# Kernel optimization log

Measured on AMD Instinct MI355X. Metric: run time of the kernel, lower is better.

The kernel has to match this reference:

```python
import jax, jax.numpy as jnp
import numpy as np

N_NODES = 100000
NEG_SLOPE = 0.2  # PyG GATConv default


def gat_conv(x, src, dst, W, a_src, a_dst, n_nodes):
    """One PyG-style GATConv (with self-loops already appended to src/dst).
    x: [N, Fin], W: [Fin, H*C], a_src/a_dst: [H, C]. Returns [N, H, C]."""
    H, C = a_src.shape
    h = (x @ W).reshape(-1, H, C)                      # [N, H, C]
    s_src = jnp.einsum('nhc,hc->nh', h, a_src)         # [N, H]
    s_dst = jnp.einsum('nhc,hc->nh', h, a_dst)         # [N, H]
    e = jax.nn.leaky_relu(s_src[src] + s_dst[dst], NEG_SLOPE)  # [E, H]
    # segment softmax over incoming edges of each destination node
    e_max = jax.ops.segment_max(e, dst, num_segments=n_nodes)  # [N, H]
    e_exp = jnp.exp(e - e_max[dst])
    denom = jax.ops.segment_sum(e_exp, dst, num_segments=n_nodes)
    alpha = e_exp / (denom[dst] + 1e-16)               # [E, H]
    msg = h[src] * alpha[:, :, None]                   # [E, H, C]
    return jax.ops.segment_sum(msg, dst, num_segments=n_nodes)  # [N, H, C]


def setup_inputs() -> dict:
    key = jax.random.key(0)
    ks = jax.random.split(key, 10)
    in_dim, hidden, heads, out_dim = 128, 32, 4, 32
    N, E = N_NODES, 1600000
    x = jax.random.normal(ks[0], (N, in_dim), dtype=jnp.float32)
    edge_index = jax.random.randint(ks[1], (2, E), 0, N, dtype=jnp.int64)
    s = 0.1
    return {
        'x': x,
        'edge_index': edge_index,
        'W1': s * jax.random.normal(ks[2], (in_dim, heads * hidden), dtype=jnp.float32),
        'a_src1': s * jax.random.normal(ks[3], (heads, hidden), dtype=jnp.float32),
        'a_dst1': s * jax.random.normal(ks[4], (heads, hidden), dtype=jnp.float32),
        'b1': jnp.zeros((heads * hidden,), dtype=jnp.float32),
        'W2': s * jax.random.normal(ks[5], (heads * hidden, out_dim), dtype=jnp.float32),
        'a_src2': s * jax.random.normal(ks[6], (1, out_dim), dtype=jnp.float32),
        'a_dst2': s * jax.random.normal(ks[7], (1, out_dim), dtype=jnp.float32),
        'b2': jnp.zeros((out_dim,), dtype=jnp.float32),
    }


def reference(x, edge_index, W1, a_src1, a_dst1, b1, W2, a_src2, a_dst2, b2):
    N = x.shape[0]
    loops = jnp.arange(N, dtype=edge_index.dtype)
    src = jnp.concatenate([edge_index[0], loops])  # PyG adds self-loops
    dst = jnp.concatenate([edge_index[1], loops])
    h1 = gat_conv(x, src, dst, W1, a_src1, a_dst1, N)      # [N, H, C]
    h1 = jax.nn.elu(h1.reshape(N, -1) + b1)                # concat heads + bias, elu
    h2 = gat_conv(h1, src, dst, W2, a_src2, a_dst2, N)     # [N, 1, out]
    return h2.mean(axis=1) + b2                            # concat=False -> mean over heads
```

## Files before the change

kernel.cpp:

```cpp
#include <hip/hip_runtime.h>
#include <hip/hip_bf16.h>

#define NEG 0.2f
#define BK_SHIFT 9
#define BK_CAP 9216

typedef short short8 __attribute__((ext_vector_type(8)));
typedef float f32x4 __attribute__((ext_vector_type(4)));

__device__ __forceinline__ float lrelu(float x){ return x > 0.f ? x : NEG * x; }
__device__ __forceinline__ float elu_f(float x){ return x > 0.f ? x : expm1f(x); }
__device__ __forceinline__ unsigned short f2bf(float f){
  unsigned int u = __float_as_uint(f);
  unsigned int r = u + 0x7fffu + ((u >> 16) & 1u);
  return (unsigned short)(r >> 16);
}
__device__ __forceinline__ float bf2f(unsigned short u){
  return __uint_as_float(((unsigned int)u) << 16);
}

__global__ __launch_bounds__(256) void k_binA(
    const int* __restrict__ src, const int* __restrict__ dst, int E,
    int* __restrict__ gcursor, int2* __restrict__ ebuf){
  __shared__ int hist[256];
  __shared__ int base[256];
  int t = threadIdx.x;
  hist[t] = 0;
  __syncthreads();
  int e0 = blockIdx.x * 4096;
  for (int j = 0; j < 16; j++){
    int e = e0 + j * 256 + t;
    if (e < E) atomicAdd(&hist[dst[e] >> BK_SHIFT], 1);
  }
  __syncthreads();
  int cnt = hist[t];
  if (cnt > 0) base[t] = atomicAdd(&gcursor[t], cnt);
  hist[t] = 0;
  __syncthreads();
  for (int j = 0; j < 16; j++){
    int e = e0 + j * 256 + t;
    if (e < E){
      int d = dst[e]; int b = d >> BK_SHIFT;
      int loc = atomicAdd(&hist[b], 1);
      ebuf[(size_t)b * BK_CAP + base[b] + loc] = make_int2(src[e], d);
    }
  }
}

__global__ __launch_bounds__(256) void k_degB(
    const int2* __restrict__ ebuf, const int* __restrict__ gcount,
    int* __restrict__ deg, int N){
  __shared__ int ld[512];
  int b = blockIdx.x, t = threadIdx.x;
  ld[t] = 0; ld[t + 256] = 0;
  __syncthreads();
  int cnt = gcount[b];
  int nbase = b << BK_SHIFT;
  const int2* eb = ebuf + (size_t)b * BK_CAP;
  for (int i = t; i < cnt; i += 256)
    atomicAdd(&ld[eb[i].y - nbase], 1);
  __syncthreads();
  int n0 = nbase + t;
  if (n0 < N) deg[n0] = ld[t];
  int n1 = nbase + 256 + t;
  if (n1 < N) deg[n1] = ld[t + 256];
}

__global__ void k_scan1(const int* __restrict__ deg, int* row_ptr, int* partials, int N){
  __shared__ int sd[256];
  int t = threadIdx.x;
  int base = blockIdx.x * 1024 + t * 4;
  int v[4]; int s = 0;
  #pragma unroll
  for (int j = 0; j < 4; j++){ int i = base + j; v[j] = (i < N) ? (deg[i] + 1) : 0; s += v[j]; }
  sd[t] = s; __syncthreads();
  for (int off = 1; off < 256; off <<= 1){
    int x = (t >= off) ? sd[t - off] : 0;
    __syncthreads(); sd[t] += x; __syncthreads();
  }
  int pre = (t > 0) ? sd[t - 1] : 0;
  #pragma unroll
  for (int j = 0; j < 4; j++){ int i = base + j; if (i < N) row_ptr[i] = pre; pre += v[j]; }
  if (t == 255) partials[blockIdx.x] = sd[255];
}

__global__ void k_scan2(int* partials, int NB){
  __shared__ int sd[128];
  int t = threadIdx.x;
  int v = (t < NB) ? partials[t] : 0;
  sd[t] = v; __syncthreads();
  for (int off = 1; off < 128; off <<= 1){
    int x = (t >= off) ? sd[t - off] : 0;
    __syncthreads(); sd[t] += x; __syncthreads();
  }
  if (t < NB) partials[t] = sd[t] - v;
}

__global__ void k_scan3(int* row_ptr, const int* __restrict__ partials, int N, int total){
  int i = blockIdx.x * blockDim.x + threadIdx.x;
  if (i < N){ int r = row_ptr[i] + partials[i >> 10]; row_ptr[i] = r; }
  if (i == 0) row_ptr[N] = total;
}

__global__ __launch_bounds__(256) void k_csrB(
    const int2* __restrict__ ebuf, const int* __restrict__ gcount,
    const int* __restrict__ rowp, int* __restrict__ csr, int N){
  __shared__ int cur[512];
  int b = blockIdx.x, t = threadIdx.x;
  int nbase = b << BK_SHIFT;
  int n0 = nbase + t;
  int n1 = nbase + 256 + t;
  cur[t]       = (n0 < N) ? rowp[n0] : 0;
  cur[t + 256] = (n1 < N) ? rowp[n1] : 0;
  __syncthreads();
  int cnt = gcount[b];
  const int2* eb = ebuf + (size_t)b * BK_CAP;
  for (int i = t; i < cnt; i += 256){
    int2 e = eb[i];
    int pos = atomicAdd(&cur[e.y - nbase], 1);
    csr[pos] = e.x;
  }
  __syncthreads();
  if (n0 < N) csr[cur[t]] = n0;
  if (n1 < N) csr[cur[t + 256]] = n1;
}

__global__ __launch_bounds__(256, 3) void k_gemm1(
    const float* __restrict__ x, const float* __restrict__ W,
    unsigned short* __restrict__ h_bf, int N){
  __shared__ unsigned short Wt[128 * 136];
  __shared__ unsigned short Xb[64 * 136];
  int t = threadIdx.x;
  int rb = blockIdx.x * 64;

  {
    int n = t & 127, kh = (t >> 7) << 6;
    #pragma unroll
    for (int j = 0; j < 16; j++){
      int k0 = kh + j * 4;
      float w0 = W[(size_t)(k0 + 0) * 128 + n];
      float w1 = W[(size_t)(k0 + 1) * 128 + n];
      float w2 = W[(size_t)(k0 + 2) * 128 + n];
      float w3 = W[(size_t)(k0 + 3) * 128 + n];
      uint2 pk;
      pk.x = ((unsigned)f2bf(w1) << 16) | f2bf(w0);
      pk.y = ((unsigned)f2bf(w3) << 16) | f2bf(w2);
      *(uint2*)&Wt[n * 136 + k0] = pk;
    }
  }
  #pragma unroll
  for (int j = 0; j < 8; j++){
    int fi = j * 256 + t;
    int row = fi >> 5, k4 = (fi & 31) * 4;
    int gr = rb + row;
    float4 v = make_float4(0.f, 0.f, 0.f, 0.f);
    if (gr < N) v = *(const float4*)&x[(size_t)gr * 128 + k4];
    uint2 pk;
    pk.x = ((unsigned)f2bf(v.y) << 16) | f2bf(v.x);
    pk.y = ((unsigned)f2bf(v.w) << 16) | f2bf(v.z);
    *(uint2*)&Xb[row * 136 + k4] = pk;
  }
  __syncthreads();

  int w = t >> 6, l = t & 63;
  int m = l & 15, quad = l >> 4;
  f32x4 acc[8];
  #pragma unroll
  for (int ct = 0; ct < 8; ct++) acc[ct] = (f32x4){0.f, 0.f, 0.f, 0.f};

  #pragma unroll
  for (int kc = 0; kc < 4; kc++){
    short8 a = *(const short8*)&Xb[(w * 16 + m) * 136 + kc * 32 + quad * 8];
    #pragma unroll
    for (int ct = 0; ct < 8; ct++){
      short8 b = *(const short8*)&Wt[(ct * 16 + m) * 136 + kc * 32 + quad * 8];
      acc[ct] = __builtin_amdgcn_mfma_f32_16x16x32_bf16(a, b, acc[ct], 0, 0, 0);
    }
  }

  #pragma unroll
  for (int reg = 0; reg < 4; reg++){
    int gr = rb + w * 16 + quad * 4 + reg;
    if (gr < N){
      #pragma unroll
      for (int ct = 0; ct < 8; ct++)
        h_bf[(size_t)gr * 128 + ct * 16 + m] = f2bf(acc[ct][reg]);
    }
  }
}

__global__ __launch_bounds__(256) void k_score1(
    const unsigned int* __restrict__ hb, const float* __restrict__ a_src,
    const float* __restrict__ a_dst, float* __restrict__ ss, float* __restrict__ sd, int N){
  int n = blockIdx.x * 4 + (threadIdx.x >> 6);
  if (n >= N) return;
  int l = threadIdx.x & 63;
  unsigned int u = hb[(size_t)n * 64 + l];
  float vx = bf2f((unsigned short)(u & 0xffff));
  float vy = bf2f((unsigned short)(u >> 16));
  float ps = vx * a_src[2 * l] + vy * a_src[2 * l + 1];
  float pd = vx * a_dst[2 * l] + vy * a_dst[2 * l + 1];
  ps += __shfl_xor(ps, 1, 16); ps += __shfl_xor(ps, 2, 16);
  ps += __shfl_xor(ps, 4, 16); ps += __shfl_xor(ps, 8, 16);
  pd += __shfl_xor(pd, 1, 16); pd += __shfl_xor(pd, 2, 16);
  pd += __shfl_xor(pd, 4, 16); pd += __shfl_xor(pd, 8, 16);
  if ((l & 15) == 0){
    int hd = l >> 4;
    ss[(size_t)n * 4 + hd] = ps;
    sd[(size_t)n * 4 + hd] = pd;
  }
}

__global__ __launch_bounds__(256) void k_agg1(
    const int* __restrict__ row_ptr, const int* __restrict__ csr_src,
    const float* __restrict__ ss, const float* __restrict__ sdst,
    const __hip_bfloat162* __restrict__ hb2,
    unsigned int* __restrict__ out1_bf, int N){
  int n = blockIdx.x * 4 + (threadIdx.x >> 6);
  if (n >= N) return;
  int l = threadIdx.x & 63;
  int hd = l >> 4;
  int j4 = l & 3;
  int hh = (l >> 2) & 3;
  float swv = sdst[(size_t)n * 4 + hh];
  float sdv = sdst[(size_t)n * 4 + hd];
  int beg = row_ptr[n], end = row_ptr[n + 1];
  float ax = 0.f, ay = 0.f, sw = 0.f;
  int e = beg;
  for (; e + 4 <= end; e += 4){
    int sj = csr_src[e + j4];
    float wv = __expf(lrelu(ss[(size_t)sj * 4 + hh] + swv));
    int s0 = __shfl(sj, 0, 4), s1 = __shfl(sj, 1, 4);
    int s2 = __shfl(sj, 2, 4), s3 = __shfl(sj, 3, 4);
    float w0 = __shfl(wv, hd * 4 + 0, 16), w1 = __shfl(wv, hd * 4 + 1, 16);
    float w2 = __shfl(wv, hd * 4 + 2, 16), w3 = __shfl(wv, hd * 4 + 3, 16);
    float2 v0 = __bfloat1622float2(hb2[(size_t)s0 * 64 + l]);
    float2 v1 = __bfloat1622float2(hb2[(size_t)s1 * 64 + l]);
    float2 v2 = __bfloat1622float2(hb2[(size_t)s2 * 64 + l]);
    float2 v3 = __bfloat1622float2(hb2[(size_t)s3 * 64 + l]);
    ax += w0*v0.x + w1*v1.x + w2*v2.x + w3*v3.x;
    ay += w0*v0.y + w1*v1.y + w2*v2.y + w3*v3.y;
    sw += w0 + w1 + w2 + w3;
  }
  for (; e < end; e++){
    int s = csr_src[e];
    float w = __expf(lrelu(ss[(size_t)s * 4 + hd] + sdv));
    float2 v = __bfloat1622float2(hb2[(size_t)s * 64 + l]);
    ax += w*v.x; ay += w*v.y; sw += w;
  }
  float inv = 1.f / (sw + 1e-16f);
  unsigned int lo = f2bf(ax * inv), hi = f2bf(ay * inv);
  out1_bf[(size_t)n * 64 + l] = (hi << 16) | lo;
}

__global__ __launch_bounds__(256) void k_gemm2(
    const unsigned int* __restrict__ out1_bf, const float* __restrict__ b1,
    const float* __restrict__ W2,
    const float* __restrict__ a_src, const float* __restrict__ a_dst,
    unsigned short* __restrict__ h2_bf, float* __restrict__ s_src2, float* __restrict__ s_dst2, int N){
  __shared__ __align__(16) float Wl[128 * 32];
  __shared__ __align__(16) float Xl[64 * 132];
  int t = threadIdx.x;
  int rb = blockIdx.x * 64;

  const float4* Wg4 = (const float4*)W2;
  float4* Wl4 = (float4*)Wl;
  #pragma unroll
  for (int j = 0; j < 4; j++) Wl4[j * 256 + t] = Wg4[j * 256 + t];

  #pragma unroll
  for (int j = 0; j < 4; j++){
    int fi = j * 256 + t;
    int row = fi >> 4, q = fi & 15;
    int gr = rb + row;
    float v[8] = {0.f,0.f,0.f,0.f,0.f,0.f,0.f,0.f};
    if (gr < N){
      uint4 u = *(const uint4*)&out1_bf[(size_t)gr * 64 + q * 4];
      float4 bva = *(const float4*)&b1[q * 8];
      float4 bvb = *(const float4*)&b1[q * 8 + 4];
      v[0] = elu_f(bf2f((unsigned short)(u.x & 0xffff)) + bva.x);
      v[1] = elu_f(bf2f((unsigned short)(u.x >> 16))    + bva.y);
      v[2] = elu_f(bf2f((unsigned short)(u.y & 0xffff)) + bva.z);
      v[3] = elu_f(bf2f((unsigned short)(u.y >> 16))    + bva.w);
      v[4] = elu_f(bf2f((unsigned short)(u.z & 0xffff)) + bvb.x);
      v[5] = elu_f(bf2f((unsigned short)(u.z >> 16))    + bvb.y);
      v[6] = elu_f(bf2f((unsigned short)(u.w & 0xffff)) + bvb.z);
      v[7] = elu_f(bf2f((unsigned short)(u.w >> 16))    + bvb.w);
    }
    #pragma unroll
    for (int i = 0; i < 8; i++) Xl[row * 132 + q * 8 + i] = v[i];
  }
  __syncthreads();

  int cg = t & 7, rg = t >> 3;
  int c0 = cg * 4, r0 = rg * 2;
  float acc[2][4] = {};

  #pragma unroll 8
  for (int k = 0; k < 128; k++){
    float a0 = Xl[r0 * 132 + k];
    float a1 = Xl[(r0 + 1) * 132 + k];
    float4 b = *(float4*)&Wl[k * 32 + c0];
    acc[0][0] += a0 * b.x; acc[0][1] += a0 * b.y; acc[0][2] += a0 * b.z; acc[0][3] += a0 * b.w;
    acc[1][0] += a1 * b.x; acc[1][1] += a1 * b.y; acc[1][2] += a1 * b.z; acc[1][3] += a1 * b.w;
  }

  float as[4], ad[4];
  #pragma unroll
  for (int j = 0; j < 4; j++){ as[j] = a_src[c0 + j]; ad[j] = a_dst[c0 + j]; }
  #pragma unroll
  for (int i = 0; i < 2; i++){
    int row = rb + r0 + i;
    if (row < N){
      ushort4 o;
      o.x = f2bf(acc[i][0]); o.y = f2bf(acc[i][1]); o.z = f2bf(acc[i][2]); o.w = f2bf(acc[i][3]);
      *(ushort4*)&h2_bf[(size_t)row * 32 + c0] = o;
    }
    float ps = 0.f, pd = 0.f;
    #pragma unroll
    for (int j = 0; j < 4; j++){ ps += acc[i][j] * as[j]; pd += acc[i][j] * ad[j]; }
    ps += __shfl_xor(ps, 1, 8); ps += __shfl_xor(ps, 2, 8); ps += __shfl_xor(ps, 4, 8);
    pd += __shfl_xor(pd, 1, 8); pd += __shfl_xor(pd, 2, 8); pd += __shfl_xor(pd, 4, 8);
    if ((t & 7) == 0 && row < N){ s_src2[row] = ps; s_dst2[row] = pd; }
  }
}

__global__ __launch_bounds__(256) void k_agg2(
    const int* __restrict__ row_ptr, const int* __restrict__ csr_src,
    const float* __restrict__ ss2, const float* __restrict__ sd2,
    const unsigned short* __restrict__ h2bf, const float* __restrict__ b2,
    float* __restrict__ out, int N){
  int n = blockIdx.x * 8 + (threadIdx.x >> 5);
  if (n >= N) return;
  int c = threadIdx.x & 31;
  float sdv = sd2[n];
  int beg = row_ptr[n], end = row_ptr[n + 1];
  float acc = 0.f, sw = 0.f;
  int e = beg;
  for (; e + 4 <= end; e += 4){
    int s0 = csr_src[e], s1 = csr_src[e+1], s2 = csr_src[e+2], s3 = csr_src[e+3];
    int sj = csr_src[e + (c & 3)];
    float wv = __expf(lrelu(ss2[sj] + sdv));
    float w0 = __shfl(wv, 0, 4), w1 = __shfl(wv, 1, 4);
    float w2 = __shfl(wv, 2, 4), w3 = __shfl(wv, 3, 4);
    float v0 = bf2f(h2bf[(size_t)s0 * 32 + c]);
    float v1 = bf2f(h2bf[(size_t)s1 * 32 + c]);
    float v2 = bf2f(h2bf[(size_t)s2 * 32 + c]);
    float v3 = bf2f(h2bf[(size_t)s3 * 32 + c]);
    acc += w0*v0 + w1*v1 + w2*v2 + w3*v3;
    sw += w0 + w1 + w2 + w3;
  }
  for (; e < end; e++){
    int s = csr_src[e];
    float w = __expf(lrelu(ss2[s] + sdv));
    acc += w * bf2f(h2bf[(size_t)s * 32 + c]);
    sw += w;
  }
  out[(size_t)n * 32 + c] = acc / (sw + 1e-16f) + b2[c];
}

extern "C" void kernel_launch(void* const* d_in, const int* in_sizes, int n_in,
                              void* d_out, int out_size, void* d_ws, size_t ws_size,
                              hipStream_t stream) {
  const float* x      = (const float*)d_in[0];
  const int*   ei     = (const int*)  d_in[1];
  const float* W1     = (const float*)d_in[2];
  const float* a_src1 = (const float*)d_in[3];
  const float* a_dst1 = (const float*)d_in[4];
  const float* b1     = (const float*)d_in[5];
  const float* W2     = (const float*)d_in[6];
  const float* a_src2 = (const float*)d_in[7];
  const float* a_dst2 = (const float*)d_in[8];
  const float* b2     = (const float*)d_in[9];
  float* out = (float*)d_out;

  int N = in_sizes[0] / 128;
  int E = in_sizes[1] / 2;
  const int* srcp = ei;
  const int* dstp = ei + E;
  int total = E + N;
  int NBK = (N + 511) >> 9;

  char* p = (char*)d_ws;
  auto alloc = [&](size_t bytes) -> void* {
    void* r = (void*)p; p += (bytes + 255) & ~(size_t)255; return r;
  };
  unsigned short* h_bf    = (unsigned short*)alloc((size_t)N * 128 * 2);
  unsigned int*   out1_bf = (unsigned int*)alloc((size_t)N * 64 * 4);
  unsigned short* h2_bf   = (unsigned short*)alloc((size_t)N * 32 * 2);
  float* ss1  = (float*)alloc((size_t)N * 4 * 4);
  float* sd1  = (float*)alloc((size_t)N * 4 * 4);
  float* ss2  = (float*)alloc((size_t)N * 4);
  float* sd2  = (float*)alloc((size_t)N * 4);
  int* deg    = (int*)alloc((size_t)N * 4);
  int* rowp   = (int*)alloc((size_t)(N + 1) * 4);
  int* csr    = (int*)alloc((size_t)total * 4);
  int* parts  = (int*)alloc(256 * 4);
  int* gcur   = (int*)alloc(256 * 4);
  int2* ebuf  = (int2*)out1_bf;
  (void)ws_size; (void)n_in; (void)out_size;

  hipMemsetAsync(gcur, 0, 256 * 4, stream);
  k_binA<<<(E + 4095) / 4096, 256, 0, stream>>>(srcp, dstp, E, gcur, ebuf);
  k_degB<<<NBK, 256, 0, stream>>>(ebuf, gcur, deg, N);
  int NB = (N + 1023) / 1024;
  k_scan1<<<NB, 256, 0, stream>>>(deg, rowp, parts, N);
  k_scan2<<<1, 128, 0, stream>>>(parts, NB);
  k_scan3<<<(N + 255) / 256, 256, 0, stream>>>(rowp, parts, N, total);
  k_csrB<<<NBK, 256, 0, stream>>>(ebuf, gcur, rowp, csr, N);

  k_gemm1<<<(N + 63) / 64, 256, 0, stream>>>(x, W1, h_bf, N);
  k_score1<<<(N + 3) / 4, 256, 0, stream>>>((const unsigned int*)h_bf, a_src1, a_dst1, ss1, sd1, N);
  k_agg1<<<(N + 3) / 4, 256, 0, stream>>>(rowp, csr, ss1, sd1, (const __hip_bfloat162*)h_bf, out1_bf, N);
  k_gemm2<<<(N + 63) / 64, 256, 0, stream>>>(out1_bf, b1, W2, a_src2, a_dst2, h2_bf, ss2, sd2, N);
  k_agg2<<<(N + 7) / 8, 256, 0, stream>>>(rowp, csr, ss2, sd2, h2_bf, b2, out, N);
}
```

Baseline: 344.8 us.

## Fuse CSR build scans per bucket, fold score1 into gemm1, widen agg1 unroll

The CSR construction drops the separate degree, three-pass scan and CSR kernels. It uses one single-block scan over bucket totals, and each bucket block then computes its own local degree histogram, prefix and row pointers before scattering. Attention scores for layer 1 are now computed in the gemm1 epilogue from the fp32 accumulators, which removes the k_score1 kernel and its re-read of h. k_agg1 gains an 8-edge unrolled loop to raise memory-level parallelism for the gathers. Together these cut launches and global traffic, at the cost of more registers in gemm1 and agg1. Scores now come from fp32 values rather than bf16-rounded ones, so results can differ slightly.

```diff
diff --git a/kernel.cpp b/kernel.cpp
--- a/kernel.cpp
+++ b/kernel.cpp
@@ -47,87 +47,69 @@
   }
 }
 
-__global__ __launch_bounds__(256) void k_degB(
-    const int2* __restrict__ ebuf, const int* __restrict__ gcount,
-    int* __restrict__ deg, int N){
-  __shared__ int ld[512];
-  int b = blockIdx.x, t = threadIdx.x;
-  ld[t] = 0; ld[t + 256] = 0;
-  __syncthreads();
-  int cnt = gcount[b];
-  int nbase = b << BK_SHIFT;
-  const int2* eb = ebuf + (size_t)b * BK_CAP;
-  for (int i = t; i < cnt; i += 256)
-    atomicAdd(&ld[eb[i].y - nbase], 1);
-  __syncthreads();
-  int n0 = nbase + t;
-  if (n0 < N) deg[n0] = ld[t];
-  int n1 = nbase + 256 + t;
-  if (n1 < N) deg[n1] = ld[t + 256];
-}
-
-__global__ void k_scan1(const int* __restrict__ deg, int* row_ptr, int* partials, int N){
+__global__ __launch_bounds__(256) void k_bscan(
+    const int* __restrict__ gcount, int* __restrict__ bbase,
+    int* __restrict__ rowp, int N, int NBK, int total){
   __shared__ int sd[256];
   int t = threadIdx.x;
-  int base = blockIdx.x * 1024 + t * 4;
-  int v[4]; int s = 0;
-  #pragma unroll
-  for (int j = 0; j < 4; j++){ int i = base + j; v[j] = (i < N) ? (deg[i] + 1) : 0; s += v[j]; }
-  sd[t] = s; __syncthreads();
+  int nodes = 0;
+  if (t < NBK){ int nb = N - (t << BK_SHIFT); nodes = nb > 512 ? 512 : nb; }
+  int v = (t < NBK) ? gcount[t] + nodes : 0;
+  sd[t] = v; __syncthreads();
   for (int off = 1; off < 256; off <<= 1){
     int x = (t >= off) ? sd[t - off] : 0;
     __syncthreads(); sd[t] += x; __syncthreads();
   }
-  int pre = (t > 0) ? sd[t - 1] : 0;
-  #pragma unroll
-  for (int j = 0; j < 4; j++){ int i = base + j; if (i < N) row_ptr[i] = pre; pre += v[j]; }
-  if (t == 255) partials[blockIdx.x] = sd[255];
-}
-
-__global__ void k_scan2(int* partials, int NB){
-  __shared__ int sd[128];
-  int t = threadIdx.x;
-  int v = (t < NB) ? partials[t] : 0;
-  sd[t] = v; __syncthreads();
-  for (int off = 1; off < 128; off <<= 1){
-    int x = (t >= off) ? sd[t - off] : 0;
-    __syncthreads(); sd[t] += x; __syncthreads();
-  }
-  if (t < NB) partials[t] = sd[t] - v;
-}
-
-__global__ void k_scan3(int* row_ptr, const int* __restrict__ partials, int N, int total){
-  int i = blockIdx.x * blockDim.x + threadIdx.x;
-  if (i < N){ int r = row_ptr[i] + partials[i >> 10]; row_ptr[i] = r; }
-  if (i == 0) row_ptr[N] = total;
-}
-
-__global__ __launch_bounds__(256) void k_csrB(
+  if (t < NBK) bbase[t] = sd[t] - v;
+  if (t == 0) rowp[N] = total;
+}
+
+__global__ __launch_bounds__(256) void k_csrB2(
     const int2* __restrict__ ebuf, const int* __restrict__ gcount,
-    const int* __restrict__ rowp, int* __restrict__ csr, int N){
-  __shared__ int cur[512];
+    const int* __restrict__ bbase, int* __restrict__ rowp,
+    int* __restrict__ csr, int N){
+  __shared__ int hist[512];
+  __shared__ int psum[256];
   int b = blockIdx.x, t = threadIdx.x;
   int nbase = b << BK_SHIFT;
-  int n0 = nbase + t;
-  int n1 = nbase + 256 + t;
-  cur[t]       = (n0 < N) ? rowp[n0] : 0;
-  cur[t + 256] = (n1 < N) ? rowp[n1] : 0;
-  __syncthreads();
   int cnt = gcount[b];
   const int2* eb = ebuf + (size_t)b * BK_CAP;
+  hist[t] = 0; hist[t + 256] = 0;
+  __syncthreads();
+  for (int i = t; i < cnt; i += 256)
+    atomicAdd(&hist[eb[i].y - nbase], 1);
+  __syncthreads();
+  int v0 = hist[2 * t], v1 = hist[2 * t + 1];
+  int ps = v0 + v1;
+  psum[t] = ps; __syncthreads();
+  for (int off = 1; off < 256; off <<= 1){
+    int x = (t >= off) ? psum[t - off] : 0;
+    __syncthreads(); psum[t] += x; __syncthreads();
+  }
+  int eo = psum[t] - ps;
+  int bb = bbase[b];
+  int n0 = 2 * t, n1 = 2 * t + 1;
+  int r0 = bb + eo + n0;
+  int r1 = bb + eo + v0 + n1;
+  if (nbase + n0 < N) rowp[nbase + n0] = r0;
+  if (nbase + n1 < N) rowp[nbase + n1] = r1;
+  __syncthreads();
+  hist[n0] = r0; hist[n1] = r1;
+  __syncthreads();
   for (int i = t; i < cnt; i += 256){
     int2 e = eb[i];
-    int pos = atomicAdd(&cur[e.y - nbase], 1);
+    int pos = atomicAdd(&hist[e.y - nbase], 1);
     csr[pos] = e.x;
   }
   __syncthreads();
-  if (n0 < N) csr[cur[t]] = n0;
-  if (n1 < N) csr[cur[t + 256]] = n1;
+  if (nbase + n0 < N) csr[hist[n0]] = nbase + n0;
+  if (nbase + n1 < N) csr[hist[n1]] = nbase + n1;
 }
 
 __global__ __launch_bounds__(256, 3) void k_gemm1(
     const float* __restrict__ x, const float* __restrict__ W,
-    unsigned short* __restrict__ h_bf, int N){
+    const float* __restrict__ a_src, const float* __restrict__ a_dst,
+    unsigned short* __restrict__ h_bf, float* __restrict__ ss, float* __restrict__ sd, int N){
   __shared__ unsigned short Wt[128 * 136];
   __shared__ unsigned short Xb[64 * 136];
   int t = threadIdx.x;
@@ -178,36 +160,29 @@
     }
   }
 
+  float as[8], ad[8];
+  #pragma unroll
+  for (int ct = 0; ct < 8; ct++){ as[ct] = a_src[ct * 16 + m]; ad[ct] = a_dst[ct * 16 + m]; }
+
   #pragma unroll
   for (int reg = 0; reg < 4; reg++){
     int gr = rb + w * 16 + quad * 4 + reg;
-    if (gr < N){
+    bool ok = gr < N;
+    if (ok){
       #pragma unroll
       for (int ct = 0; ct < 8; ct++)
         h_bf[(size_t)gr * 128 + ct * 16 + m] = f2bf(acc[ct][reg]);
     }
-  }
-}
-
-__global__ __launch_bounds__(256) void k_score1(
-    const unsigned int* __restrict__ hb, const float* __restrict__ a_src,
-    const float* __restrict__ a_dst, float* __restrict__ ss, float* __restrict__ sd, int N){
-  int n = blockIdx.x * 4 + (threadIdx.x >> 6);
-  if (n >= N) return;
-  int l = threadIdx.x & 63;
-  unsigned int u = hb[(size_t)n * 64 + l];
-  float vx = bf2f((unsigned short)(u & 0xffff));
-  float vy = bf2f((unsigned short)(u >> 16));
-  float ps = vx * a_src[2 * l] + vy * a_src[2 * l + 1];
-  float pd = vx * a_dst[2 * l] + vy * a_dst[2 * l + 1];
-  ps += __shfl_xor(ps, 1, 16); ps += __shfl_xor(ps, 2, 16);
-  ps += __shfl_xor(ps, 4, 16); ps += __shfl_xor(ps, 8, 16);
-  pd += __shfl_xor(pd, 1, 16); pd += __shfl_xor(pd, 2, 16);
-  pd += __shfl_xor(pd, 4, 16); pd += __shfl_xor(pd, 8, 16);
-  if ((l & 15) == 0){
-    int hd = l >> 4;
-    ss[(size_t)n * 4 + hd] = ps;
-    sd[(size_t)n * 4 + hd] = pd;
+    #pragma unroll
+    for (int hh = 0; hh < 4; hh++){
+      float ps = acc[2*hh][reg] * as[2*hh] + acc[2*hh+1][reg] * as[2*hh+1];
+      float pd = acc[2*hh][reg] * ad[2*hh] + acc[2*hh+1][reg] * ad[2*hh+1];
+      ps += __shfl_xor(ps, 1, 16); ps += __shfl_xor(ps, 2, 16);
+      ps += __shfl_xor(ps, 4, 16); ps += __shfl_xor(ps, 8, 16);
+      pd += __shfl_xor(pd, 1, 16); pd += __shfl_xor(pd, 2, 16);
+      pd += __shfl_xor(pd, 4, 16); pd += __shfl_xor(pd, 8, 16);
+      if (m == 0 && ok){ ss[(size_t)gr * 4 + hh] = ps; sd[(size_t)gr * 4 + hh] = pd; }
+    }
   }
 }
 
@@ -220,16 +195,38 @@
   if (n >= N) return;
   int l = threadIdx.x & 63;
   int hd = l >> 4;
-  int j4 = l & 3;
-  int hh = (l >> 2) & 3;
-  float swv = sdst[(size_t)n * 4 + hh];
   float sdv = sdst[(size_t)n * 4 + hd];
+  int j8 = l & 7, hh8 = (l >> 3) & 3;
+  float sw8 = sdst[(size_t)n * 4 + hh8];
+  int j4 = l & 3, hh4 = (l >> 2) & 3;
+  float sw4 = sdst[(size_t)n * 4 + hh4];
   int beg = row_ptr[n], end = row_ptr[n + 1];
   float ax = 0.f, ay = 0.f, sw = 0.f;
   int e = beg;
+  for (; e + 8 <= end; e += 8){
+    int sj = csr_src[e + j8];
+    float wv = __expf(lrelu(ss[(size_t)sj * 4 + hh8] + sw8));
+    int s0 = __shfl(sj, 0, 8), s1 = __shfl(sj, 1, 8), s2 = __shfl(sj, 2, 8), s3 = __shfl(sj, 3, 8);
+    int s4 = __shfl(sj, 4, 8), s5 = __shfl(sj, 5, 8), s6 = __shfl(sj, 6, 8), s7 = __shfl(sj, 7, 8);
+    float w0 = __shfl(wv, hd * 8 + 0, 32), w1 = __shfl(wv, hd * 8 + 1, 32);
+    float w2 = __shfl(wv, hd * 8 + 2, 32), w3 = __shfl(wv, hd * 8 + 3, 32);
+    float w4 = __shfl(wv, hd * 8 + 4, 32), w5 = __shfl(wv, hd * 8 + 5, 32);
+    float w6 = __shfl(wv, hd * 8 + 6, 32), w7 = __shfl(wv, hd * 8 + 7, 32);
+    float2 v0 = __bfloat1622float2(hb2[(size_t)s0 * 64 + l]);
+    float2 v1 = __bfloat1622float2(hb2[(size_t)s1 * 64 + l]);
+    float2 v2 = __bfloat1622float2(hb2[(size_t)s2 * 64 + l]);
+    float2 v3 = __bfloat1622float2(hb2[(size_t)s3 * 64 + l]);
+    float2 v4 = __bfloat1622float2(hb2[(size_t)s4 * 64 + l]);
+    float2 v5 = __bfloat1622float2(hb2[(size_t)s5 * 64 + l]);
+    float2 v6 = __bfloat1622float2(hb2[(size_t)s6 * 64 + l]);
+    float2 v7 = __bfloat1622float2(hb2[(size_t)s7 * 64 + l]);
+    ax += w0*v0.x + w1*v1.x + w2*v2.x + w3*v3.x + w4*v4.x + w5*v5.x + w6*v6.x + w7*v7.x;
+    ay += w0*v0.y + w1*v1.y + w2*v2.y + w3*v3.y + w4*v4.y + w5*v5.y + w6*v6.y + w7*v7.y;
+    sw += w0 + w1 + w2 + w3 + w4 + w5 + w6 + w7;
+  }
   for (; e + 4 <= end; e += 4){
     int sj = csr_src[e + j4];
-    float wv = __expf(lrelu(ss[(size_t)sj * 4 + hh] + swv));
+    float wv = __expf(lrelu(ss[(size_t)sj * 4 + hh4] + sw4));
     int s0 = __shfl(sj, 0, 4), s1 = __shfl(sj, 1, 4);
     int s2 = __shfl(sj, 2, 4), s3 = __shfl(sj, 3, 4);
     float w0 = __shfl(wv, hd * 4 + 0, 16), w1 = __shfl(wv, hd * 4 + 1, 16);
@@ -392,25 +389,19 @@
   float* sd1  = (float*)alloc((size_t)N * 4 * 4);
   float* ss2  = (float*)alloc((size_t)N * 4);
   float* sd2  = (float*)alloc((size_t)N * 4);
-  int* deg    = (int*)alloc((size_t)N * 4);
   int* rowp   = (int*)alloc((size_t)(N + 1) * 4);
   int* csr    = (int*)alloc((size_t)total * 4);
-  int* parts  = (int*)alloc(256 * 4);
+  int* bbase  = (int*)alloc(256 * 4);
   int* gcur   = (int*)alloc(256 * 4);
   int2* ebuf  = (int2*)out1_bf;
   (void)ws_size; (void)n_in; (void)out_size;
 
   hipMemsetAsync(gcur, 0, 256 * 4, stream);
   k_binA<<<(E + 4095) / 4096, 256, 0, stream>>>(srcp, dstp, E, gcur, ebuf);
-  k_degB<<<NBK, 256, 0, stream>>>(ebuf, gcur, deg, N);
-  int NB = (N + 1023) / 1024;
-  k_scan1<<<NB, 256, 0, stream>>>(deg, rowp, parts, N);
-  k_scan2<<<1, 128, 0, stream>>>(parts, NB);
-  k_scan3<<<(N + 255) / 256, 256, 0, stream>>>(rowp, parts, N, total);
-  k_csrB<<<NBK, 256, 0, stream>>>(ebuf, gcur, rowp, csr, N);
-
-  k_gemm1<<<(N + 63) / 64, 256, 0, stream>>>(x, W1, h_bf, N);
-  k_score1<<<(N + 3) / 4, 256, 0, stream>>>((const unsigned int*)h_bf, a_src1, a_dst1, ss1, sd1, N);
+  k_bscan<<<1, 256, 0, stream>>>(gcur, bbase, rowp, N, NBK, total);
+  k_csrB2<<<NBK, 256, 0, stream>>>(ebuf, gcur, bbase, rowp, csr, N);
+
+  k_gemm1<<<(N + 63) / 64, 256, 0, stream>>>(x, W1, a_src1, a_dst1, h_bf, ss1, sd1, N);
   k_agg1<<<(N + 3) / 4, 256, 0, stream>>>(rowp, csr, ss1, sd1, (const __hip_bfloat162*)h_bf, out1_bf, N);
   k_gemm2<<<(N + 63) / 64, 256, 0, stream>>>(out1_bf, b1, W2, a_src2, a_dst2, h2_bf, ss2, sd2, N);
   k_agg2<<<(N + 7) / 8, 256, 0, stream>>>(rowp, csr, ss2, sd2, h2_bf, b2, out, N);
```

Result: faster. 331.2 us (-4.0%).
